# Performance work log

Measured on AMD Instinct MI355X. Metric: run time of the kernel, lower is better.

## Reference

```python
import jax, jax.numpy as jnp
import numpy as np

HEADS = 8
EPS = 1e-5


def layernorm(x, g, b):
    mu = jnp.mean(x, axis=-1, keepdims=True)
    var = jnp.mean((x - mu) ** 2, axis=-1, keepdims=True)
    return (x - mu) * jax.lax.rsqrt(var + EPS) * g + b


def setup_inputs() -> dict:
    key = jax.random.key(0)
    ks = jax.random.split(key, 5)
    B, C, H, W = 8, 384, 32, 32
    d = C
    s = 0.02
    return {
        "x": jax.random.normal(ks[0], (B, C, H, W), jnp.float32),
        "ln1_g": jnp.ones((d,), jnp.float32),
        "ln1_b": jnp.zeros((d,), jnp.float32),
        "lna_g": jnp.ones((d,), jnp.float32),
        "lna_b": jnp.zeros((d,), jnp.float32),
        "w_qkv": jax.random.normal(ks[1], (d, 3 * d), jnp.float32) * s,
        "w_out": jax.random.normal(ks[2], (d, d), jnp.float32) * s,
        "ln2_g": jnp.ones((d,), jnp.float32),
        "ln2_b": jnp.zeros((d,), jnp.float32),
        "w1": jax.random.normal(ks[3], (d, 4 * d), jnp.float32) * s,
        "b1": jnp.zeros((4 * d,), jnp.float32),
        "w2": jax.random.normal(ks[4], (4 * d, d), jnp.float32) * s,
        "b2": jnp.zeros((d,), jnp.float32),
    }


def reference(x, ln1_g, ln1_b, lna_g, lna_b, w_qkv, w_out, ln2_g, ln2_b, w1, b1, w2, b2):
    B, C, H, W = x.shape
    d = C
    dh = d // HEADS
    scale = dh ** (-0.5)
    # flatten spatial -> tokens: [B, N, C]
    t = x.reshape(B, C, H * W).transpose(0, 2, 1)

    # --- attention branch (note: double pre-norm, as in original) ---
    a = layernorm(t, ln1_g, ln1_b)
    a = layernorm(a, lna_g, lna_b)
    qkv = a @ w_qkv  # [B, N, 3d]
    q, k, v = jnp.split(qkv, 3, axis=-1)
    q = q.reshape(B, -1, HEADS, dh).transpose(0, 2, 1, 3)  # b h n d
    k = k.reshape(B, -1, HEADS, dh).transpose(0, 2, 1, 3)
    v = v.reshape(B, -1, HEADS, dh).transpose(0, 2, 1, 3)
    dots = jnp.einsum("bhnd,bhmd->bhnm", q, k) * scale
    attn = jax.nn.softmax(dots, axis=-1)
    o = jnp.einsum("bhnm,bhmd->bhnd", attn, v)
    o = o.transpose(0, 2, 1, 3).reshape(B, -1, d)
    t = t + o @ w_out

    # --- MLP branch (exact GELU, as torch nn.GELU default) ---
    m = layernorm(t, ln2_g, ln2_b)
    m = jax.nn.gelu(m @ w1 + b1, approximate=False) @ w2 + b2
    t = t + m

    return t.transpose(0, 2, 1).reshape(B, C, H, W)
```

## Files before the change

### kernel.cpp

```cpp
#include <hip/hip_runtime.h>
#include <math.h>

#define NTOK 1024
#define DM   384
#define NHEAD 8
#define DH   48
#define BATCH 8
#define NROWS (BATCH * NTOK)
#define SC2   (0.14433756729740643f * 1.4426950408889634f)

typedef __attribute__((ext_vector_type(8))) _Float16 f16x8;
typedef __attribute__((ext_vector_type(2))) __fp16 fp16x2_raw;
typedef __attribute__((ext_vector_type(4))) float f32x4;

#define ASYNC16(gp, lp) __builtin_amdgcn_global_load_lds( \
    (const __attribute__((address_space(1))) void*)(gp),  \
    (__attribute__((address_space(3))) void*)(lp), 16, 0, 0)

#define EXP2R(x) __builtin_amdgcn_exp2f(x)
#define RCPR(x)  __builtin_amdgcn_rcpf(x)

__device__ __forceinline__ unsigned int pkh(float a, float b) {
    union { fp16x2_raw h; unsigned int u; } cv;
    cv.h = __builtin_amdgcn_cvt_pkrtz(a, b);
    return cv.u;
}

__device__ __forceinline__ float gelu_fast(float v) {
    const float u = v * (0.7978845608f + 0.0356774081f * v * v);
    const float e = EXP2R(fminf(u * 2.885390082f, 120.0f));
    return v * e * RCPR(e + 1.0f);
}

__global__ __launch_bounds__(256) void prep_kernel(const float* __restrict__ x,
                                                   const float* __restrict__ ln1_g,
                                                   const float* __restrict__ ln1_b,
                                                   const float* __restrict__ lna_g,
                                                   const float* __restrict__ lna_b,
                                                   float* __restrict__ t,
                                                   _Float16* __restrict__ a_h,
                                                   const float* __restrict__ wqkv,
                                                   const float* __restrict__ wout,
                                                   const float* __restrict__ w1,
                                                   const float* __restrict__ w2,
                                                   _Float16* __restrict__ wqkvT,
                                                   _Float16* __restrict__ woutT,
                                                   _Float16* __restrict__ w1T,
                                                   _Float16* __restrict__ w2T) {
    __shared__ float Ts[32][389];
    const int bid = blockIdx.x;
    const int tid = threadIdx.x;

    if (bid >= 256) {
        float (*tile)[33] = (float(*)[33])&Ts[0][0];
        const int wb = bid - 256;
        const float* W; _Float16* Wt; int K, N, nx, tt;
        if (wb < 432)       { W = wqkv; Wt = wqkvT; K = 384;  N = 1152; nx = 36; tt = wb; }
        else if (wb < 576)  { W = wout; Wt = woutT; K = 384;  N = 384;  nx = 12; tt = wb - 432; }
        else if (wb < 1152) { W = w1;   Wt = w1T;   K = 384;  N = 1536; nx = 48; tt = wb - 576; }
        else                { W = w2;   Wt = w2T;   K = 1536; N = 384;  nx = 12; tt = wb - 1152; }
        const int n0 = (tt % nx) * 32, k0 = (tt / nx) * 32;
        const int tx = tid & 31, ty = tid >> 5;
        #pragma unroll
        for (int i = ty; i < 32; i += 8)
            tile[i][tx] = W[(size_t)(k0 + i) * N + n0 + tx];
        __syncthreads();
        #pragma unroll
        for (int i = ty; i < 32; i += 8)
            Wt[(size_t)(n0 + i) * K + k0 + tx] = (_Float16)tile[tx][i];
        return;
    }

    const int b = bid >> 5, n0 = (bid & 31) * 32;
    const int tx = tid & 31, ty8 = tid >> 5;
    const float* xb = x + (size_t)b * (DM * NTOK);
    #pragma unroll
    for (int c0 = 0; c0 < DM; c0 += 32) {
        #pragma unroll
        for (int i = ty8; i < 32; i += 8)
            Ts[tx][c0 + i] = xb[(size_t)(c0 + i) * NTOK + n0 + tx];
    }
    __syncthreads();

    const int g = tid >> 3, sub = tid & 7;
    const int c0 = sub * 48;
    float xv[48];
    #pragma unroll
    for (int k = 0; k < 12; ++k)
        *(float4*)&xv[k * 4] = *(const float4*)&Ts[g][c0 + k * 4];

    const size_t trow = (size_t)((b << 10) + n0 + g) * DM;
    float s = 0.0f, sq = 0.0f;
    #pragma unroll
    for (int k = 0; k < 12; ++k)
        *(float4*)&t[trow + c0 + k * 4] = *(const float4*)&xv[k * 4];
    #pragma unroll
    for (int j = 0; j < 48; ++j) { s += xv[j]; sq += xv[j] * xv[j]; }
    s += __shfl_xor(s, 1, 64); sq += __shfl_xor(sq, 1, 64);
    s += __shfl_xor(s, 2, 64); sq += __shfl_xor(sq, 2, 64);
    s += __shfl_xor(s, 4, 64); sq += __shfl_xor(sq, 4, 64);
    float mu = s * (1.0f / DM);
    float var = fmaxf(sq * (1.0f / DM) - mu * mu, 0.0f);
    float r1 = rsqrtf(var + 1e-5f);

    float s2 = 0.0f, q2 = 0.0f;
    #pragma unroll
    for (int k = 0; k < 12; ++k) {
        const float4 gk = *(const float4*)&ln1_g[c0 + k * 4];
        const float4 bk = *(const float4*)&ln1_b[c0 + k * 4];
        float y0 = (xv[k*4+0] - mu) * r1 * gk.x + bk.x;
        float y1 = (xv[k*4+1] - mu) * r1 * gk.y + bk.y;
        float y2 = (xv[k*4+2] - mu) * r1 * gk.z + bk.z;
        float y3 = (xv[k*4+3] - mu) * r1 * gk.w + bk.w;
        xv[k*4+0] = y0; xv[k*4+1] = y1; xv[k*4+2] = y2; xv[k*4+3] = y3;
        s2 += (y0 + y1) + (y2 + y3);
        q2 += (y0*y0 + y1*y1) + (y2*y2 + y3*y3);
    }
    s2 += __shfl_xor(s2, 1, 64); q2 += __shfl_xor(q2, 1, 64);
    s2 += __shfl_xor(s2, 2, 64); q2 += __shfl_xor(q2, 2, 64);
    s2 += __shfl_xor(s2, 4, 64); q2 += __shfl_xor(q2, 4, 64);
    mu = s2 * (1.0f / DM);
    var = fmaxf(q2 * (1.0f / DM) - mu * mu, 0.0f);
    const float r2 = rsqrtf(var + 1e-5f);

    unsigned int d[12];
    #pragma unroll
    for (int k = 0; k < 12; ++k) {
        const float4 gk = *(const float4*)&lna_g[c0 + k * 4];
        const float4 bk = *(const float4*)&lna_b[c0 + k * 4];
        const float y0 = (xv[k*4+0] - mu) * r2 * gk.x + bk.x;
        const float y1 = (xv[k*4+1] - mu) * r2 * gk.y + bk.y;
        const float y2 = (xv[k*4+2] - mu) * r2 * gk.z + bk.z;
        const float y3 = (xv[k*4+3] - mu) * r2 * gk.w + bk.w;
        d[k*2+0] = pkh(y0, y1); d[k*2+1] = pkh(y2, y3);
    }
    unsigned int* op = (unsigned int*)(a_h + trow + c0);
    #pragma unroll
    for (int k = 0; k < 3; ++k)
        *(uint4*)(op + k * 4) = *(const uint4*)&d[k * 4];
}

__global__ __launch_bounds__(256) void ln2_kernel(const float* __restrict__ in,
                                                  const float* __restrict__ gg,
                                                  const float* __restrict__ bb,
                                                  _Float16* __restrict__ outp) {
    const int row = blockIdx.x * 4 + (threadIdx.x >> 6);
    const int lane = threadIdx.x & 63;
    const float* ip = in + (size_t)row * DM + lane * 6;
    float v[6];
    *(float2*)&v[0] = *(const float2*)(ip);
    *(float2*)&v[2] = *(const float2*)(ip + 2);
    *(float2*)&v[4] = *(const float2*)(ip + 4);
    float s = 0.0f, sq = 0.0f;
    #pragma unroll
    for (int j = 0; j < 6; ++j) { s += v[j]; sq += v[j] * v[j]; }
    #pragma unroll
    for (int off = 1; off < 64; off <<= 1) {
        s += __shfl_xor(s, off, 64);
        sq += __shfl_xor(sq, off, 64);
    }
    const float mu = s * (1.0f / DM);
    const float var = fmaxf(sq * (1.0f / DM) - mu * mu, 0.0f);
    const float rs = rsqrtf(var + 1e-5f);
    const float* gp = gg + lane * 6;
    const float* bp = bb + lane * 6;
    float y[6];
    #pragma unroll
    for (int j = 0; j < 6; ++j) y[j] = (v[j] - mu) * rs * gp[j] + bp[j];
    unsigned int* op = (unsigned int*)(outp + (size_t)row * DM + lane * 6);
    op[0] = pkh(y[0], y[1]); op[1] = pkh(y[2], y[3]); op[2] = pkh(y[4], y[5]);
}

template <int EPI, int BN>
__global__ __launch_bounds__(256) void gemm_f16(const _Float16* __restrict__ A,
                                                const _Float16* __restrict__ Bt,
                                                const float* __restrict__ bias,
                                                const float* __restrict__ R,
                                                _Float16* __restrict__ Ch,
                                                float* __restrict__ Cf,
                                                int M, int N, int K) {
    constexpr int NFRAG = BN / 32;
    __shared__ _Float16 As[128][64];
    __shared__ _Float16 Bs[BN][64];
    const int tid = threadIdx.x;
    const int w = tid >> 6, lane = tid & 63;
    const int l15 = lane & 15, lq = lane >> 4;
    const int bm = blockIdx.y * 128, bn = blockIdx.x * BN;
    const int moff = (w & 1) * 64, noff = (w >> 1) * (BN / 2);

    const int srw = lane >> 3, pp = lane & 7;
    const int c = pp ^ srw;
    const _Float16* Ag[4];
    const _Float16* Bg[BN / 32];
    #pragma unroll
    for (int j = 0; j < 4; ++j)
        Ag[j] = A + (size_t)(bm + w * 32 + j * 8 + srw) * K + c * 8;
    #pragma unroll
    for (int j = 0; j < BN / 32; ++j)
        Bg[j] = Bt + (size_t)(bn + w * (BN / 4) + j * 8 + srw) * K + c * 8;

    const int octA = ((lq ^ (l15 & 7)) << 4);

    f32x4 acc[4][NFRAG];
    #pragma unroll
    for (int mi = 0; mi < 4; ++mi)
        #pragma unroll
        for (int ni = 0; ni < NFRAG; ++ni) acc[mi][ni] = (f32x4){0.f, 0.f, 0.f, 0.f};

    for (int k0 = 0; k0 < K; k0 += 64) {
        __syncthreads();
        #pragma unroll
        for (int j = 0; j < 4; ++j) {
            ASYNC16(Ag[j], &As[w * 32 + j * 8][0]);
            Ag[j] += 64;
        }
        #pragma unroll
        for (int j = 0; j < BN / 32; ++j) {
            ASYNC16(Bg[j], &Bs[w * (BN / 4) + j * 8][0]);
            Bg[j] += 64;
        }
        __syncthreads();
        #pragma unroll
        for (int ks = 0; ks < 2; ++ks) {
            const int ox = octA ^ (ks << 6);
            f16x8 af[4], bfr[NFRAG];
            #pragma unroll
            for (int mi = 0; mi < 4; ++mi)
                af[mi] = *(const f16x8*)((const char*)As + ((moff + mi * 16 + l15) << 7) + ox);
            #pragma unroll
            for (int ni = 0; ni < NFRAG; ++ni)
                bfr[ni] = *(const f16x8*)((const char*)Bs + ((noff + ni * 16 + l15) << 7) + ox);
            #pragma unroll
            for (int mi = 0; mi < 4; ++mi)
                #pragma unroll
                for (int ni = 0; ni < NFRAG; ++ni)
                    acc[mi][ni] = __builtin_amdgcn_mfma_f32_16x16x32_f16(af[mi], bfr[ni], acc[mi][ni], 0, 0, 0);
        }
    }

    #pragma unroll
    for (int mi = 0; mi < 4; ++mi) {
        #pragma unroll
        for (int ni = 0; ni < NFRAG; ++ni) {
            const int col = bn + noff + ni * 16 + l15;
            float bv = 0.0f;
            if (EPI >= 2) bv = bias[col];
            if (EPI == 4) {
                const int row0 = bm + moff + mi * 16 + lq * 4;
                const int b = row0 >> 10, nn = row0 & 1023;
                float4 vv;
                vv.x = acc[mi][ni][0] + bv + R[(size_t)(row0 + 0) * N + col];
                vv.y = acc[mi][ni][1] + bv + R[(size_t)(row0 + 1) * N + col];
                vv.z = acc[mi][ni][2] + bv + R[(size_t)(row0 + 2) * N + col];
                vv.w = acc[mi][ni][3] + bv + R[(size_t)(row0 + 3) * N + col];
                *(float4*)(Cf + (size_t)b * (DM * NTOK) + (size_t)col * NTOK + nn) = vv;
            } else {
                #pragma unroll
                for (int r = 0; r < 4; ++r) {
                    const int row = bm + moff + mi * 16 + lq * 4 + r;
                    const size_t idx = (size_t)row * N + col;
                    float v = acc[mi][ni][r];
                    if (EPI == 2) v = gelu_fast(v + bv);
                    if (EPI == 0 || EPI == 2) Ch[idx] = (_Float16)v;
                    else                      Cf[idx] = v + R[idx];
                }
            }
        }
    }
}

__global__ __launch_bounds__(256) void attn_kernel(const _Float16* __restrict__ qkv,
                                                   _Float16* __restrict__ o) {
    __shared__ _Float16 Ks[2][64][64];
    __shared__ _Float16 Vt[2][48][72];
    __shared__ _Float16 Ps[4][16][72];
    const int tid = threadIdx.x;
    const int w = tid >> 6, lane = tid & 63;
    const int l15 = lane & 15, lq = lane >> 4;
    const int bid = blockIdx.x;
    const int bh = ((bid >> 3) & 7) * 8 + (bid & 7);
    const int qt0 = (bid >> 6) * 64;
    const int h = bh & 7, b = bh >> 3;

    const _Float16* qbase = qkv + (size_t)b * NTOK * 1152 + h * 48;
    const _Float16* kbase = qbase + 384;
    const _Float16* vbase = qbase + 768;

    f16x8 qf[2];
    {
        const size_t qrow = (size_t)(qt0 + w * 16 + l15) * 1152;
        qf[0] = *(const f16x8*)(qbase + qrow + lq * 8);
        if (lq < 2) qf[1] = *(const f16x8*)(qbase + qrow + 32 + lq * 8);
        else        qf[1] = (f16x8){(_Float16)0, (_Float16)0, (_Float16)0, (_Float16)0,
                                    (_Float16)0, (_Float16)0, (_Float16)0, (_Float16)0};
    }

    const int srw = lane >> 3, pp = lane & 7;
    const int ck = pp ^ srw;
    const int ckoff = (ck < 6) ? ck * 8 : (ck - 6) * 8;
    const _Float16* Kg = kbase + (size_t)(w * 16 + srw) * 1152 + ckoff;
    const int vtp = tid & 31, vfo = tid >> 5;
    const _Float16* Vg = vbase + (size_t)(vtp * 2) * 1152 + vfo * 8;

    const int octK = ((lq ^ (l15 & 7)) << 4);

    ASYNC16(Kg, &Ks[0][w * 16][0]);
    ASYNC16(Kg + 8 * 1152, &Ks[0][w * 16 + 8][0]);
    Kg += 64 * 1152;
    uint4 va, vb;
    if (vfo < 6) { va = *(const uint4*)Vg; vb = *(const uint4*)(Vg + 1152); }
    Vg += 64 * 1152;

    f32x4 oacc[3];
    float lpart = 0.0f;
    #pragma unroll
    for (int vf = 0; vf < 3; ++vf) oacc[vf] = (f32x4){0.f, 0.f, 0.f, 0.f};

    int cur = 0;
    for (int kt = 0; kt < 16; ++kt) {
        if (vfo < 6) {
            const unsigned short* as = (const unsigned short*)&va;
            const unsigned short* bs = (const unsigned short*)&vb;
            #pragma unroll
            for (int j = 0; j < 8; ++j) {
                const unsigned int dw = (unsigned int)as[j] | ((unsigned int)bs[j] << 16);
                *(unsigned int*)((char*)&Vt[cur][0][0] + (vfo * 8 + j) * 144 + vtp * 4) = dw;
            }
        }
        __syncthreads();
        if (kt < 15) {
            ASYNC16(Kg, &Ks[cur ^ 1][w * 16][0]);
            ASYNC16(Kg + 8 * 1152, &Ks[cur ^ 1][w * 16 + 8][0]);
            Kg += 64 * 1152;
            if (vfo < 6) { va = *(const uint4*)Vg; vb = *(const uint4*)(Vg + 1152); }
            Vg += 64 * 1152;
        }

        f32x4 sacc[4];
        #pragma unroll
        for (int mi = 0; mi < 4; ++mi) sacc[mi] = (f32x4){0.f, 0.f, 0.f, 0.f};
        #pragma unroll
        for (int ks = 0; ks < 2; ++ks) {
            const int ox = octK ^ (ks << 6);
            #pragma unroll
            for (int mi = 0; mi < 4; ++mi) {
                const f16x8 kf = *(const f16x8*)((const char*)&Ks[cur][0][0] + ((mi * 16 + l15) << 7) + ox);
                sacc[mi] = __builtin_amdgcn_mfma_f32_16x16x32_f16(kf, qf[ks], sacc[mi], 0, 0, 0);
            }
        }

        #pragma unroll
        for (int mi = 0; mi < 4; ++mi) {
            const float p0 = EXP2R(sacc[mi][0] * SC2);
            const float p1 = EXP2R(sacc[mi][1] * SC2);
            const float p2 = EXP2R(sacc[mi][2] * SC2);
            const float p3 = EXP2R(sacc[mi][3] * SC2);
            lpart += (p0 + p1) + (p2 + p3);
            uint2 d;
            d.x = pkh(p0, p1); d.y = pkh(p2, p3);
            *(uint2*)((char*)&Ps[w][0][0] + l15 * 144 + (mi * 16 + lq * 4) * 2) = d;
        }
        asm volatile("s_waitcnt lgkmcnt(0)" ::: "memory");

        #pragma unroll
        for (int ks = 0; ks < 2; ++ks) {
            const int kk2 = ks * 64 + lq * 16;
            const f16x8 pf = *(const f16x8*)((const char*)&Ps[w][0][0] + l15 * 144 + kk2);
            #pragma unroll
            for (int vf = 0; vf < 3; ++vf) {
                const f16x8 vv = *(const f16x8*)((const char*)&Vt[cur][0][0] + (vf * 16 + l15) * 144 + kk2);
                oacc[vf] = __builtin_amdgcn_mfma_f32_16x16x32_f16(vv, pf, oacc[vf], 0, 0, 0);
            }
        }
        cur ^= 1;
    }

    lpart += __shfl_xor(lpart, 16, 64);
    lpart += __shfl_xor(lpart, 32, 64);
    const float linv = RCPR(lpart);
    _Float16* ob = o + (size_t)(b * NTOK + qt0 + w * 16 + l15) * DM + h * DH;
    #pragma unroll
    for (int vf = 0; vf < 3; ++vf) {
        uint2 d;
        d.x = pkh(oacc[vf][0] * linv, oacc[vf][1] * linv);
        d.y = pkh(oacc[vf][2] * linv, oacc[vf][3] * linv);
        *(uint2*)(ob + vf * 16 + lq * 4) = d;
    }
}

extern "C" void kernel_launch(void* const* d_in, const int* in_sizes, int n_in,
                              void* d_out, int out_size, void* d_ws, size_t ws_size,
                              hipStream_t stream) {
    const float* x     = (const float*)d_in[0];
    const float* ln1_g = (const float*)d_in[1];
    const float* ln1_b = (const float*)d_in[2];
    const float* lna_g = (const float*)d_in[3];
    const float* lna_b = (const float*)d_in[4];
    const float* w_qkv = (const float*)d_in[5];
    const float* w_out = (const float*)d_in[6];
    const float* ln2_g = (const float*)d_in[7];
    const float* ln2_b = (const float*)d_in[8];
    const float* w1    = (const float*)d_in[9];
    const float* b1    = (const float*)d_in[10];
    const float* w2    = (const float*)d_in[11];
    const float* b2    = (const float*)d_in[12];
    float* out = (float*)d_out;

    char* wsb = (char*)d_ws;
    float* t          = (float*)(wsb);
    _Float16* a_h     = (_Float16*)(wsb + 12582912);
    _Float16* qkv_h   = (_Float16*)(wsb + 18874368);
    _Float16* o_h     = (_Float16*)(wsb + 37748736);
    _Float16* h1_h    = (_Float16*)(wsb + 44040192);
    _Float16* wqkvT   = (_Float16*)(wsb + 69206016);
    _Float16* woutT   = (_Float16*)(wsb + 70090752);
    _Float16* w1T     = (_Float16*)(wsb + 70385664);
    _Float16* w2T     = (_Float16*)(wsb + 71565312);

    prep_kernel<<<256 + 1728, 256, 0, stream>>>(x, ln1_g, ln1_b, lna_g, lna_b, t, a_h,
                                                w_qkv, w_out, w1, w2, wqkvT, woutT, w1T, w2T);
    gemm_f16<0, 128><<<dim3(9, 64), 256, 0, stream>>>(a_h, wqkvT, nullptr, nullptr, qkv_h, nullptr, NROWS, 3 * DM, DM);
    attn_kernel<<<1024, 256, 0, stream>>>(qkv_h, o_h);
    gemm_f16<1, 64><<<dim3(6, 64), 256, 0, stream>>>(o_h, woutT, nullptr, t, nullptr, t, NROWS, DM, DM);
    ln2_kernel<<<2048, 256, 0, stream>>>(t, ln2_g, ln2_b, a_h);
    gemm_f16<2, 128><<<dim3(12, 64), 256, 0, stream>>>(a_h, w1T, b1, nullptr, h1_h, nullptr, NROWS, 4 * DM, DM);
    gemm_f16<4, 64><<<dim3(6, 64), 256, 0, stream>>>(h1_h, w2T, b2, t, nullptr, out, NROWS, DM, 4 * DM);
}
```

Measured before the change: 229.1 us.

## Fuse out-projection GEMM with residual add and LayerNorm2

Replaces the out-projection GEMM plus separate ln2 kernel with one kernel in which each block computes full 384-wide rows (32 rows per block), adds the residual, and computes row mean and variance with a cross-wave reduction in shared memory. It then writes both the updated residual stream and the normalized fp16 activations. This removes one launch and a full read of t for the second LayerNorm. In exchange the grid shrinks to 256 blocks, each using a large shared-memory B tile (about 100KB double-buffered), which may lower occupancy and reload the weight matrix once per block.

```diff
diff --git a/kernel.cpp b/kernel.cpp
--- a/kernel.cpp
+++ b/kernel.cpp
@@ -138,37 +138,6 @@
     #pragma unroll
     for (int k = 0; k < 3; ++k)
         *(uint4*)(op + k * 4) = *(const uint4*)&d[k * 4];
-}
-
-__global__ __launch_bounds__(256) void ln2_kernel(const float* __restrict__ in,
-                                                  const float* __restrict__ gg,
-                                                  const float* __restrict__ bb,
-                                                  _Float16* __restrict__ outp) {
-    const int row = blockIdx.x * 4 + (threadIdx.x >> 6);
-    const int lane = threadIdx.x & 63;
-    const float* ip = in + (size_t)row * DM + lane * 6;
-    float v[6];
-    *(float2*)&v[0] = *(const float2*)(ip);
-    *(float2*)&v[2] = *(const float2*)(ip + 2);
-    *(float2*)&v[4] = *(const float2*)(ip + 4);
-    float s = 0.0f, sq = 0.0f;
-    #pragma unroll
-    for (int j = 0; j < 6; ++j) { s += v[j]; sq += v[j] * v[j]; }
-    #pragma unroll
-    for (int off = 1; off < 64; off <<= 1) {
-        s += __shfl_xor(s, off, 64);
-        sq += __shfl_xor(sq, off, 64);
-    }
-    const float mu = s * (1.0f / DM);
-    const float var = fmaxf(sq * (1.0f / DM) - mu * mu, 0.0f);
-    const float rs = rsqrtf(var + 1e-5f);
-    const float* gp = gg + lane * 6;
-    const float* bp = bb + lane * 6;
-    float y[6];
-    #pragma unroll
-    for (int j = 0; j < 6; ++j) y[j] = (v[j] - mu) * rs * gp[j] + bp[j];
-    unsigned int* op = (unsigned int*)(outp + (size_t)row * DM + lane * 6);
-    op[0] = pkh(y[0], y[1]); op[1] = pkh(y[2], y[3]); op[2] = pkh(y[4], y[5]);
 }
 
 template <int EPI, int BN>
@@ -261,10 +230,115 @@
                     const size_t idx = (size_t)row * N + col;
                     float v = acc[mi][ni][r];
                     if (EPI == 2) v = gelu_fast(v + bv);
-                    if (EPI == 0 || EPI == 2) Ch[idx] = (_Float16)v;
-                    else                      Cf[idx] = v + R[idx];
+                    Ch[idx] = (_Float16)v;
                 }
             }
+        }
+    }
+}
+
+__global__ __launch_bounds__(256) void gemm_out_ln(const _Float16* __restrict__ A,
+                                                   const _Float16* __restrict__ Bt,
+                                                   float* __restrict__ T,
+                                                   _Float16* __restrict__ a_out,
+                                                   const float* __restrict__ gg,
+                                                   const float* __restrict__ bb) {
+    __shared__ _Float16 As[2][32][64];
+    __shared__ _Float16 Bs[2][384][64];
+    __shared__ float red_s[4][16];
+    __shared__ float red_q[4][16];
+    const int tid = threadIdx.x;
+    const int w = tid >> 6, lane = tid & 63;
+    const int l15 = lane & 15, lq = lane >> 4;
+    const int bm = blockIdx.x * 32;
+    const int mr = (w & 1) * 16;
+    const int cq = (w >> 1) * 192;
+
+    const int srw = lane >> 3, pp = lane & 7;
+    const int c = pp ^ srw;
+    const _Float16* Ag = A + (size_t)(bm + w * 8 + srw) * 384 + c * 8;
+    const _Float16* Bg[12];
+    #pragma unroll
+    for (int j = 0; j < 12; ++j)
+        Bg[j] = Bt + (size_t)(j * 32 + w * 8 + srw) * 384 + c * 8;
+
+    const int octA = ((lq ^ (l15 & 7)) << 4);
+
+    f32x4 acc[12];
+    #pragma unroll
+    for (int ni = 0; ni < 12; ++ni) acc[ni] = (f32x4){0.f, 0.f, 0.f, 0.f};
+
+    ASYNC16(Ag, &As[0][w * 8][0]); Ag += 64;
+    #pragma unroll
+    for (int j = 0; j < 12; ++j) { ASYNC16(Bg[j], &Bs[0][j * 32 + w * 8][0]); Bg[j] += 64; }
+
+    for (int kt = 0; kt < 6; ++kt) {
+        const int cur = kt & 1;
+        __syncthreads();
+        if (kt < 5) {
+            ASYNC16(Ag, &As[cur ^ 1][w * 8][0]); Ag += 64;
+            #pragma unroll
+            for (int j = 0; j < 12; ++j) { ASYNC16(Bg[j], &Bs[cur ^ 1][j * 32 + w * 8][0]); Bg[j] += 64; }
+        }
+        #pragma unroll
+        for (int ks = 0; ks < 2; ++ks) {
+            const int ox = octA ^ (ks << 6);
+            const f16x8 af = *(const f16x8*)((const char*)&As[cur][0][0] + ((mr + l15) << 7) + ox);
+            #pragma unroll
+            for (int ni = 0; ni < 12; ++ni) {
+                const f16x8 bf = *(const f16x8*)((const char*)&Bs[cur][0][0] + ((cq + ni * 16 + l15) << 7) + ox);
+                acc[ni] = __builtin_amdgcn_mfma_f32_16x16x32_f16(af, bf, acc[ni], 0, 0, 0);
+            }
+        }
+    }
+
+    float vv[12][4];
+    float s[4] = {0.f, 0.f, 0.f, 0.f}, q[4] = {0.f, 0.f, 0.f, 0.f};
+    #pragma unroll
+    for (int ni = 0; ni < 12; ++ni) {
+        const int col = cq + ni * 16 + l15;
+        #pragma unroll
+        for (int r = 0; r < 4; ++r) {
+            const int row = bm + mr + lq * 4 + r;
+            const float v = acc[ni][r] + T[(size_t)row * DM + col];
+            vv[ni][r] = v;
+            T[(size_t)row * DM + col] = v;
+            s[r] += v; q[r] += v * v;
+        }
+    }
+    #pragma unroll
+    for (int off = 1; off < 16; off <<= 1) {
+        #pragma unroll
+        for (int r = 0; r < 4; ++r) {
+            s[r] += __shfl_xor(s[r], off, 64);
+            q[r] += __shfl_xor(q[r], off, 64);
+        }
+    }
+    if (l15 == 0) {
+        #pragma unroll
+        for (int r = 0; r < 4; ++r) {
+            red_s[w][lq * 4 + r] = s[r];
+            red_q[w][lq * 4 + r] = q[r];
+        }
+    }
+    __syncthreads();
+    float mu[4], rs[4];
+    #pragma unroll
+    for (int r = 0; r < 4; ++r) {
+        const float ts = s[r] + red_s[w ^ 2][lq * 4 + r];
+        const float tq = q[r] + red_q[w ^ 2][lq * 4 + r];
+        mu[r] = ts * (1.0f / DM);
+        const float var = fmaxf(tq * (1.0f / DM) - mu[r] * mu[r], 0.0f);
+        rs[r] = rsqrtf(var + 1e-5f);
+    }
+    #pragma unroll
+    for (int ni = 0; ni < 12; ++ni) {
+        const int col = cq + ni * 16 + l15;
+        const float gv = gg[col], bv = bb[col];
+        #pragma unroll
+        for (int r = 0; r < 4; ++r) {
+            const int row = bm + mr + lq * 4 + r;
+            a_out[(size_t)row * DM + col] = (_Float16)((vv[ni][r] - mu[r]) * rs[r] * gv + bv);
         }
     }
 }
@@ -421,8 +495,7 @@
                                                 w_qkv, w_out, w1, w2, wqkvT, woutT, w1T, w2T);
     gemm_f16<0, 128><<<dim3(9, 64), 256, 0, stream>>>(a_h, wqkvT, nullptr, nullptr, qkv_h, nullptr, NROWS, 3 * DM, DM);
     attn_kernel<<<1024, 256, 0, stream>>>(qkv_h, o_h);
-    gemm_f16<1, 64><<<dim3(6, 64), 256, 0, stream>>>(o_h, woutT, nullptr, t, nullptr, t, NROWS, DM, DM);
-    ln2_kernel<<<2048, 256, 0, stream>>>(t, ln2_g, ln2_b, a_h);
+    gemm_out_ln<<<256, 256, 0, stream>>>(o_h, woutT, t, a_h, ln2_g, ln2_b);
     gemm_f16<2, 128><<<dim3(12, 64), 256, 0, stream>>>(a_h, w1T, b1, nullptr, h1_h, nullptr, NROWS, 4 * DM, DM);
     gemm_f16<4, 64><<<dim3(6, 64), 256, 0, stream>>>(h1_h, w2T, b2, t, nullptr, out, NROWS, DM, 4 * DM);
 }
```

Result: no change. 225.4 us (-1.6%).
